# Performance work log

Hardware: AMD Instinct MI355X
Metric: run time of the kernel (lower is better)

## Reference

```python
import jax, jax.numpy as jnp
import numpy as np

B, P, F, H, C, D = 512, 32, 16, 4, 32, 128   # graphs, nodes/graph, node feat, heads, head_dim, hidden
N = B * P
E_DIM = 5

def _lin(k, o, i):
    return jax.random.normal(k, (o, i)) * (1.0 / np.sqrt(i))

def setup_inputs():
    key = jax.random.key(0)
    ks = jax.random.split(key, 32)
    # fully-connected directed edges (no self loops) within each graph
    a = np.repeat(np.arange(P), P); b = np.tile(np.arange(P), P)
    m = a != b; a, b = a[m], b[m]
    off = (np.arange(B) * P)[:, None]
    src = (a[None, :] + off).reshape(-1); dst = (b[None, :] + off).reshape(-1)
    edge_index = jnp.asarray(np.stack([src, dst]), dtype=jnp.int32)
    E = src.size
    x = jax.random.normal(ks[0], (N, F))
    edge_attr = jax.random.normal(ks[1], (E, E_DIM))
    z = jnp.zeros
    return dict(
        x=x, edge_index=edge_index, edge_attr=edge_attr,
        W1l=_lin(ks[2], D, F), b1l=z(D), W1r=_lin(ks[3], D, F), b1r=z(D),
        W1e=_lin(ks[4], D, E_DIM), att1=jax.random.normal(ks[5], (1, H, C)) * 0.1, bias1=z(D),
        W2l=_lin(ks[6], D, D), b2l=z(D), W2r=_lin(ks[7], D, D), b2r=z(D),
        W2e=_lin(ks[8], D, E_DIM), att2=jax.random.normal(ks[9], (1, H, C)) * 0.1, bias2=z(D),
        Wc1=_lin(ks[10], D, D), bc1=z(D), Wc2=_lin(ks[11], 1, D), bc2=z(1),
        Ws1=_lin(ks[12], D, D), bs1=z(D), Ws2=_lin(ks[13], 1, D), bs2=z(1),
        Wn1=_lin(ks[14], D, D), bn1=z(D), Wn2=_lin(ks[15], 1, D), bn2=z(1),
    )

def _gatv2(x, src, dst, edge_attr, Wl, bl, Wr, br, We, att, bias):
    # PyG GATv2Conv, concat=True, heads=H, out_channels=C, edge_dim=E_DIM, add_self_loops=False
    E = src.shape[0]
    xl = x @ Wl.T + bl                                   # [N, H*C] messages (source side)
    xr = x @ Wr.T + br                                   # [N, H*C] destination side
    e = (xl[src] + xr[dst] + edge_attr @ We.T).reshape(E, H, C)
    g = jax.nn.leaky_relu(e, 0.2)
    score = jnp.sum(g * att, axis=-1)                    # [E, H]
    smax = jax.ops.segment_max(score, dst, num_segments=N)
    ex = jnp.exp(score - smax[dst])
    denom = jax.ops.segment_sum(ex, dst, num_segments=N)
    alpha = ex / (denom[dst] + 1e-16)                    # segment softmax over in-edges of dst
    msg = xl[src].reshape(E, H, C) * alpha[..., None]
    return jax.ops.segment_sum(msg, dst, num_segments=N).reshape(N, H * C) + bias

def _mlp(h, W1, b1, W2, b2):
    return jax.nn.relu(h @ W1.T + b1) @ W2.T + b2

def reference(x, edge_index, edge_attr, W1l, b1l, W1r, b1r, W1e, att1, bias1,
              W2l, b2l, W2r, b2r, W2e, att2, bias2,
              Wc1, bc1, Wc2, bc2, Ws1, bs1, Ws2, bs2, Wn1, bn1, Wn2, bn2):
    src, dst = edge_index[0], edge_index[1]
    h = _gatv2(x, src, dst, edge_attr, W1l, b1l, W1r, b1r, W1e, att1, bias1)
    hb = h.reshape(B, P, D)
    h = (hb - hb.mean(axis=1, keepdims=True)).reshape(N, D)   # MeanSubtractionNorm per graph
    h = jax.nn.relu(h)
    h = jax.nn.relu(_gatv2(h, src, dst, edge_attr, W2l, b2l, W2r, b2r, W2e, att2, bias2))
    g = h.reshape(B, P, D).mean(axis=1)                       # global_mean_pool (equal-size graphs)
    value = _mlp(g, Wc1, bc1, Wc2, bc2)                       # critic        [B, 1]
    src_logits = _mlp(h, Ws1, bs1, Ws2, bs2).reshape(B, P)    # source_actor, dense per graph
    noop = _mlp(g, Wn1, bn1, Wn2, bn2)                        # noop_actor    [B, 1]
    return jnp.concatenate([value, noop, src_logits], axis=1) # [B, P+2]
```

## Files before the change

kernel.cpp:

```cpp
#include <hip/hip_runtime.h>

#define PP    32
#define FF    16
#define HH    4
#define CC    32
#define DD    128
#define EDIM  5
#define EPG   992
#define NB    512

template <int CTRL>
__device__ __forceinline__ float dpp_add(float v) {
    int t = __builtin_amdgcn_update_dpp(0, __builtin_bit_cast(int, v), CTRL, 0xF, 0xF, true);
    return v + __builtin_bit_cast(float, t);
}
__device__ __forceinline__ float red64(float v) {
    v = dpp_add<0x111>(v);
    v = dpp_add<0x112>(v);
    v = dpp_add<0x114>(v);
    v = dpp_add<0x118>(v);
    v = dpp_add<0x142>(v);
    v = dpp_add<0x143>(v);
    return v;
}
__device__ __forceinline__ float redquad(float v) {
    v = dpp_add<0xB1>(v);
    v = dpp_add<0x4E>(v);
    return v;
}

__device__ __forceinline__ void attention(const float* __restrict__ eattr,
                                          const float* __restrict__ We, const float* __restrict__ att,
                                          const float* __restrict__ bias,
                                          const float* __restrict__ sMsg, const float* __restrict__ sDst,
                                          float* __restrict__ sS, float* __restrict__ sOut,
                                          int tid, long eBase, bool relu)
{
    {
        const int s  = tid >> 4;
        const int ch0 = (tid & 15) * 8;
        float we[40], at[8], xl[8];
#pragma unroll
        for (int q = 0; q < 10; ++q)
            *(float4*)(we + q * 4) = *(const float4*)(We + ch0 * EDIM + q * 4);
        *(float4*)(at)     = *(const float4*)(att + ch0);
        *(float4*)(at + 4) = *(const float4*)(att + ch0 + 4);
        *(float4*)(xl)     = *(const float4*)(sMsg + s * DD + ch0);
        *(float4*)(xl + 4) = *(const float4*)(sMsg + s * DD + ch0 + 4);

        for (int d = 0; d < PP; ++d) {
            int jj = d - (d > s);
            if (jj > 30) jj = 30;
            const float* ea = eattr + (eBase + s * 31 + jj) * EDIM;
            const float e0 = ea[0], e1 = ea[1], e2 = ea[2], e3 = ea[3], e4 = ea[4];
            float xr[8];
            *(float4*)(xr)     = *(const float4*)(sDst + d * DD + ch0);
            *(float4*)(xr + 4) = *(const float4*)(sDst + d * DD + ch0 + 4);
            float acc0 = 0.f, acc1 = 0.f;
#pragma unroll
            for (int c = 0; c < 8; ++c) {
                float v = xl[c] + xr[c];
                const float* w = we + c * EDIM;
                v = fmaf(w[0], e0, v); v = fmaf(w[1], e1, v); v = fmaf(w[2], e2, v);
                v = fmaf(w[3], e3, v); v = fmaf(w[4], e4, v);
                v = fmaf(0.4f, fabsf(v), 0.6f * v);
                if (c & 1) acc1 = fmaf(v, at[c], acc1);
                else       acc0 = fmaf(v, at[c], acc0);
            }
            const float r = redquad(acc0 + acc1);
            if ((tid & 3) == 0)
                sS[s * DD + d * HH + ((tid >> 2) & 3)] = r;
        }
    }
    __syncthreads();
    if (tid < PP * HH) {
        const int d = tid >> 2;
        float mx = -3.4e38f;
#pragma unroll
        for (int s = 0; s < PP; ++s) if (s != d) mx = fmaxf(mx, sS[s * DD + tid]);
        float sum = 0.f;
#pragma unroll
        for (int s = 0; s < PP; ++s) {
            if (s != d) { float ex = __expf(sS[s * DD + tid] - mx); sS[s * DD + tid] = ex; sum += ex; }
        }
        const float inv = 1.f / (sum + 1e-16f);
#pragma unroll
        for (int s = 0; s < PP; ++s)
            sS[s * DD + tid] = (s == d) ? 0.f : sS[s * DD + tid] * inv;
    }
    __syncthreads();
    {
        const int d = tid >> 4, sub = tid & 15;
#pragma unroll
        for (int half = 0; half < 2; ++half) {
            const int ch4 = half * 16 + sub;
            const int idx = d * HH + (ch4 >> 3);
            const float* bp = bias + ch4 * 4;
            float4 acc = make_float4(bp[0], bp[1], bp[2], bp[3]);
#pragma unroll
            for (int s = 0; s < PP; ++s) {
                const float a = sS[s * DD + idx];
                const float4 xv = *(const float4*)(sMsg + s * DD + ch4 * 4);
                acc.x = fmaf(a, xv.x, acc.x);
                acc.y = fmaf(a, xv.y, acc.y);
                acc.z = fmaf(a, xv.z, acc.z);
                acc.w = fmaf(a, xv.w, acc.w);
            }
            if (relu) {
                acc.x = fmaxf(acc.x, 0.f); acc.y = fmaxf(acc.y, 0.f);
                acc.z = fmaxf(acc.z, 0.f); acc.w = fmaxf(acc.w, 0.f);
            }
            *(float4*)(sOut + d * DD + ch4 * 4) = acc;
        }
    }
}

extern "C" __global__ void __launch_bounds__(512, 4)
planetwars_gnn_kernel(const float* __restrict__ x, const float* __restrict__ eattr,
                      const float* __restrict__ W1l, const float* __restrict__ b1l,
                      const float* __restrict__ W1r, const float* __restrict__ b1r,
                      const float* __restrict__ W1e, const float* __restrict__ att1, const float* __restrict__ bias1,
                      const float* __restrict__ W2l, const float* __restrict__ b2l,
                      const float* __restrict__ W2r, const float* __restrict__ b2r,
                      const float* __restrict__ W2e, const float* __restrict__ att2, const float* __restrict__ bias2,
                      const float* __restrict__ Wc1, const float* __restrict__ bc1,
                      const float* __restrict__ Wc2, const float* __restrict__ bc2,
                      const float* __restrict__ Ws1, const float* __restrict__ bs1,
                      const float* __restrict__ Ws2, const float* __restrict__ bs2,
                      const float* __restrict__ Wn1, const float* __restrict__ bn1,
                      const float* __restrict__ Wn2, const float* __restrict__ bn2,
                      float* __restrict__ out)
{
    __shared__ __align__(16) float sA[PP * DD];
    __shared__ __align__(16) float sB[PP * DD];
    __shared__ __align__(16) float sH[PP * DD];
    __shared__ __align__(16) float sU[PP * DD];

    const int tid = threadIdx.x;
    const int g = blockIdx.x;
    const long eBase = (long)g * EPG;

    sU[tid] = x[g * PP * FF + tid];
    __syncthreads();

    {
        const int j = tid & 127, d0 = (tid >> 7) * 8;
        float wl[16], wr[16];
#pragma unroll
        for (int q = 0; q < 4; ++q) {
            *(float4*)(wl + q * 4) = *(const float4*)(W1l + j * FF + q * 4);
            *(float4*)(wr + q * 4) = *(const float4*)(W1r + j * FF + q * 4);
        }
        const float bl = b1l[j], br = b1r[j];
#pragma unroll
        for (int i = 0; i < 8; ++i) {
            const float* xr = sU + (d0 + i) * FF;
            float al = bl, ar = br;
#pragma unroll
            for (int k = 0; k < FF; ++k) {
                const float xv = xr[k];
                al = fmaf(wl[k], xv, al);
                ar = fmaf(wr[k], xv, ar);
            }
            sA[(d0 + i) * DD + j] = al;
            sB[(d0 + i) * DD + j] = ar;
        }
    }
    __syncthreads();

    attention(eattr, W1e, att1, bias1, sA, sB, sU, sH, tid, eBase, false);
    __syncthreads();

    if (tid < DD) {
        float s = 0.f;
#pragma unroll
        for (int d = 0; d < PP; ++d) s += sH[d * DD + tid];
        const float mn = s * (1.0f / 32.0f);
#pragma unroll
        for (int d = 0; d < PP; ++d)
            sH[d * DD + tid] = fmaxf(sH[d * DD + tid] - mn, 0.f);
    }
    __syncthreads();

    {
        const int jj = tid & 63, d0 = (tid >> 6) * 4;
        float accL0[4], accL1[4], accR0[4], accR1[4];
        const float bl0 = b2l[jj], bl1 = b2l[jj + 64];
        const float br0 = b2r[jj], br1 = b2r[jj + 64];
#pragma unroll
        for (int i = 0; i < 4; ++i) { accL0[i] = bl0; accL1[i] = bl1; accR0[i] = br0; accR1[i] = br1; }
        const float* WL0 = W2l + jj * DD;
        const float* WL1 = W2l + (jj + 64) * DD;
        const float* WR0 = W2r + jj * DD;
        const float* WR1 = W2r + (jj + 64) * DD;
        for (int k8 = 0; k8 < 16; ++k8) {
            const float4 l00 = *(const float4*)(WL0 + k8 * 8), l01 = *(const float4*)(WL0 + k8 * 8 + 4);
            const float4 l10 = *(const float4*)(WL1 + k8 * 8), l11 = *(const float4*)(WL1 + k8 * 8 + 4);
            const float4 r00 = *(const float4*)(WR0 + k8 * 8), r01 = *(const float4*)(WR0 + k8 * 8 + 4);
            const float4 r10 = *(const float4*)(WR1 + k8 * 8), r11 = *(const float4*)(WR1 + k8 * 8 + 4);
#pragma unroll
            for (int i = 0; i < 4; ++i) {
                const float4 a0 = *(const float4*)(sH + (d0 + i) * DD + k8 * 8);
                const float4 a1 = *(const float4*)(sH + (d0 + i) * DD + k8 * 8 + 4);
                accL0[i] = fmaf(l00.x, a0.x, accL0[i]); accL0[i] = fmaf(l00.y, a0.y, accL0[i]);
                accL0[i] = fmaf(l00.z, a0.z, accL0[i]); accL0[i] = fmaf(l00.w, a0.w, accL0[i]);
                accL0[i] = fmaf(l01.x, a1.x, accL0[i]); accL0[i] = fmaf(l01.y, a1.y, accL0[i]);
                accL0[i] = fmaf(l01.z, a1.z, accL0[i]); accL0[i] = fmaf(l01.w, a1.w, accL0[i]);
                accL1[i] = fmaf(l10.x, a0.x, accL1[i]); accL1[i] = fmaf(l10.y, a0.y, accL1[i]);
                accL1[i] = fmaf(l10.z, a0.z, accL1[i]); accL1[i] = fmaf(l10.w, a0.w, accL1[i]);
                accL1[i] = fmaf(l11.x, a1.x, accL1[i]); accL1[i] = fmaf(l11.y, a1.y, accL1[i]);
                accL1[i] = fmaf(l11.z, a1.z, accL1[i]); accL1[i] = fmaf(l11.w, a1.w, accL1[i]);
                accR0[i] = fmaf(r00.x, a0.x, accR0[i]); accR0[i] = fmaf(r00.y, a0.y, accR0[i]);
                accR0[i] = fmaf(r00.z, a0.z, accR0[i]); accR0[i] = fmaf(r00.w, a0.w, accR0[i]);
                accR0[i] = fmaf(r01.x, a1.x, accR0[i]); accR0[i] = fmaf(r01.y, a1.y, accR0[i]);
                accR0[i] = fmaf(r01.z, a1.z, accR0[i]); accR0[i] = fmaf(r01.w, a1.w, accR0[i]);
                accR1[i] = fmaf(r10.x, a0.x, accR1[i]); accR1[i] = fmaf(r10.y, a0.y, accR1[i]);
                accR1[i] = fmaf(r10.z, a0.z, accR1[i]); accR1[i] = fmaf(r10.w, a0.w, accR1[i]);
                accR1[i] = fmaf(r11.x, a1.x, accR1[i]); accR1[i] = fmaf(r11.y, a1.y, accR1[i]);
                accR1[i] = fmaf(r11.z, a1.z, accR1[i]); accR1[i] = fmaf(r11.w, a1.w, accR1[i]);
            }
        }
#pragma unroll
        for (int i = 0; i < 4; ++i) {
            sA[(d0 + i) * DD + jj]      = accL0[i];
            sA[(d0 + i) * DD + jj + 64] = accL1[i];
            sB[(d0 + i) * DD + jj]      = accR0[i];
            sB[(d0 + i) * DD + jj + 64] = accR1[i];
        }
    }
    __syncthreads();

    attention(eattr, W2e, att2, bias2, sA, sB, sU, sH, tid, eBase, true);
    __syncthreads();

    if (tid < DD) {
        float s = 0.f;
#pragma unroll
        for (int d = 0; d < PP; ++d) s += sH[d * DD + tid];
        sU[tid] = s * (1.0f / 32.0f);
    }
    __syncthreads();

    {
        const int jj = tid & 63, d0 = (tid >> 6) * 4;
        const float b0 = bs1[jj], b1 = bs1[jj + 64];
        float acc0[4], acc1[4];
#pragma unroll
        for (int i = 0; i < 4; ++i) { acc0[i] = b0; acc1[i] = b1; }
        const float* W0 = Ws1 + jj * DD;
        const float* W1 = Ws1 + (jj + 64) * DD;
        for (int k8 = 0; k8 < 16; ++k8) {
            const float4 w00 = *(const float4*)(W0 + k8 * 8), w01 = *(const float4*)(W0 + k8 * 8 + 4);
            const float4 w10 = *(const float4*)(W1 + k8 * 8), w11 = *(const float4*)(W1 + k8 * 8 + 4);
#pragma unroll
            for (int i = 0; i < 4; ++i) {
                const float4 a0 = *(const float4*)(sH + (d0 + i) * DD + k8 * 8);
                const float4 a1 = *(const float4*)(sH + (d0 + i) * DD + k8 * 8 + 4);
                acc0[i] = fmaf(w00.x, a0.x, acc0[i]); acc0[i] = fmaf(w00.y, a0.y, acc0[i]);
                acc0[i] = fmaf(w00.z, a0.z, acc0[i]); acc0[i] = fmaf(w00.w, a0.w, acc0[i]);
                acc0[i] = fmaf(w01.x, a1.x, acc0[i]); acc0[i] = fmaf(w01.y, a1.y, acc0[i]);
                acc0[i] = fmaf(w01.z, a1.z, acc0[i]); acc0[i] = fmaf(w01.w, a1.w, acc0[i]);
                acc1[i] = fmaf(w10.x, a0.x, acc1[i]); acc1[i] = fmaf(w10.y, a0.y, acc1[i]);
                acc1[i] = fmaf(w10.z, a0.z, acc1[i]); acc1[i] = fmaf(w10.w, a0.w, acc1[i]);
                acc1[i] = fmaf(w11.x, a1.x, acc1[i]); acc1[i] = fmaf(w11.y, a1.y, acc1[i]);
                acc1[i] = fmaf(w11.z, a1.z, acc1[i]); acc1[i] = fmaf(w11.w, a1.w, acc1[i]);
            }
        }
        const float ws2a = Ws2[jj], ws2b = Ws2[jj + 64];
        const float bias2s = bs2[0];
#pragma unroll
        for (int i = 0; i < 4; ++i) {
            const float t = fmaf(fmaxf(acc0[i], 0.f), ws2a, fmaxf(acc1[i], 0.f) * ws2b);
            const float r = red64(t);
            if ((tid & 63) == 63) out[g * 34 + 2 + d0 + i] = r + bias2s;
        }
    }

    if (tid < 128) {
        const int w = tid >> 6, j = tid & 63;
        const float* Wa = (w ? Wn1 : Wc1);
        const float* ba = (w ? bn1 : bc1);
        const float* Wb = (w ? Wn2 : Wc2);
        const float  bb = (w ? bn2 : bc2)[0];
        float h0 = ba[j], h1 = ba[j + 64];
        const float* R0 = Wa + j * DD;
        const float* R1 = Wa + (j + 64) * DD;
#pragma unroll
        for (int k8 = 0; k8 < 16; ++k8) {
            const float4 g0 = *(const float4*)(sU + k8 * 8);
            const float4 g1 = *(const float4*)(sU + k8 * 8 + 4);
            const float4 p00 = *(const float4*)(R0 + k8 * 8), p01 = *(const float4*)(R0 + k8 * 8 + 4);
            const float4 p10 = *(const float4*)(R1 + k8 * 8), p11 = *(const float4*)(R1 + k8 * 8 + 4);
            h0 = fmaf(p00.x, g0.x, h0); h0 = fmaf(p00.y, g0.y, h0);
            h0 = fmaf(p00.z, g0.z, h0); h0 = fmaf(p00.w, g0.w, h0);
            h0 = fmaf(p01.x, g1.x, h0); h0 = fmaf(p01.y, g1.y, h0);
            h0 = fmaf(p01.z, g1.z, h0); h0 = fmaf(p01.w, g1.w, h0);
            h1 = fmaf(p10.x, g0.x, h1); h1 = fmaf(p10.y, g0.y, h1);
            h1 = fmaf(p10.z, g0.z, h1); h1 = fmaf(p10.w, g0.w, h1);
            h1 = fmaf(p11.x, g1.x, h1); h1 = fmaf(p11.y, g1.y, h1);
            h1 = fmaf(p11.z, g1.z, h1); h1 = fmaf(p11.w, g1.w, h1);
        }
        const float t = fmaf(fmaxf(h0, 0.f), Wb[j], fmaxf(h1, 0.f) * Wb[j + 64]);
        const float r = red64(t);
        if (j == 63) out[g * 34 + w] = r + bb;
    }
}

extern "C" void kernel_launch(void* const* d_in, const int* in_sizes, int n_in,
                              void* d_out, int out_size, void* d_ws, size_t ws_size,
                              hipStream_t stream)
{
    (void)in_sizes; (void)n_in; (void)d_ws; (void)ws_size; (void)out_size;
    planetwars_gnn_kernel<<<dim3(NB), dim3(512), 0, stream>>>(
        (const float*)d_in[0], (const float*)d_in[2],
        (const float*)d_in[3], (const float*)d_in[4], (const float*)d_in[5], (const float*)d_in[6],
        (const float*)d_in[7], (const float*)d_in[8], (const float*)d_in[9],
        (const float*)d_in[10], (const float*)d_in[11], (const float*)d_in[12], (const float*)d_in[13],
        (const float*)d_in[14], (const float*)d_in[15], (const float*)d_in[16],
        (const float*)d_in[17], (const float*)d_in[18], (const float*)d_in[19], (const float*)d_in[20],
        (const float*)d_in[21], (const float*)d_in[22], (const float*)d_in[23], (const float*)d_in[24],
        (const float*)d_in[25], (const float*)d_in[26], (const float*)d_in[27], (const float*)d_in[28],
        (float*)d_out);
}
```

Measured before the change: 255.7 us.

## Spread softmax and column reductions over all threads with DPP quad reductions

The segment softmax and the per-graph column mean reductions now use all 512 threads, with 4 lanes per column each handling 8 rows and combining through DPP quad max/sum, where previously only 128 threads each walked 32 rows serially. The score loop is restructured so each lane loads edge attributes for one of 4 destinations and broadcasts them to its quad via DPP, and the next group's attributes are prefetched. This also removes the divergent lane-0-only score store. The aim is to cut idle threads and serial shared-memory loops, at the cost of more DPP ops and register pressure. One FMA order swap in the layer-2 GEMM is incidental.

```diff
diff --git a/kernel.cpp b/kernel.cpp
--- a/kernel.cpp
+++ b/kernel.cpp
@@ -14,6 +14,16 @@
     int t = __builtin_amdgcn_update_dpp(0, __builtin_bit_cast(int, v), CTRL, 0xF, 0xF, true);
     return v + __builtin_bit_cast(float, t);
 }
+template <int CTRL>
+__device__ __forceinline__ float dpp_mov(float v) {
+    int t = __builtin_amdgcn_update_dpp(0, __builtin_bit_cast(int, v), CTRL, 0xF, 0xF, true);
+    return __builtin_bit_cast(float, t);
+}
+template <int DK>
+__device__ __forceinline__ float qb(float v) {
+    int t = __builtin_amdgcn_update_dpp(0, __builtin_bit_cast(int, v), DK * 0x55, 0xF, 0xF, true);
+    return __builtin_bit_cast(float, t);
+}
 __device__ __forceinline__ float red64(float v) {
     v = dpp_add<0x111>(v);
     v = dpp_add<0x112>(v);
@@ -28,6 +38,35 @@
     v = dpp_add<0x4E>(v);
     return v;
 }
+__device__ __forceinline__ float maxquad(float v) {
+    v = fmaxf(v, dpp_mov<0xB1>(v));
+    v = fmaxf(v, dpp_mov<0x4E>(v));
+    return v;
+}
+
+template <int DK>
+__device__ __forceinline__ float score_step(const float* __restrict__ sDst, int d, int ch0,
+                                            const float* we, const float* at, const float* xl,
+                                            const float* eaC)
+{
+    const float e0 = qb<DK>(eaC[0]), e1 = qb<DK>(eaC[1]), e2 = qb<DK>(eaC[2]),
+                e3 = qb<DK>(eaC[3]), e4 = qb<DK>(eaC[4]);
+    float xr[8];
+    *(float4*)(xr)     = *(const float4*)(sDst + d * DD + ch0);
+    *(float4*)(xr + 4) = *(const float4*)(sDst + d * DD + ch0 + 4);
+    float acc0 = 0.f, acc1 = 0.f;
+#pragma unroll
+    for (int c = 0; c < 8; ++c) {
+        float v = xl[c] + xr[c];
+        const float* w = we + c * EDIM;
+        v = fmaf(w[0], e0, v); v = fmaf(w[1], e1, v); v = fmaf(w[2], e2, v);
+        v = fmaf(w[3], e3, v); v = fmaf(w[4], e4, v);
+        v = fmaf(0.4f, fabsf(v), 0.6f * v);
+        if (c & 1) acc1 = fmaf(v, at[c], acc1);
+        else       acc0 = fmaf(v, at[c], acc0);
+    }
+    return redquad(acc0 + acc1);
+}
 
 __device__ __forceinline__ void attention(const float* __restrict__ eattr,
                                           const float* __restrict__ We, const float* __restrict__ att,
@@ -37,7 +76,9 @@
                                           int tid, long eBase, bool relu)
 {
     {
-        const int s  = tid >> 4;
+        const int s   = tid >> 4;
+        const int h4  = (tid >> 2) & 3;
+        const int c4  = tid & 3;
         const int ch0 = (tid & 15) * 8;
         float we[40], at[8], xl[8];
 #pragma unroll
@@ -48,45 +89,62 @@
         *(float4*)(xl)     = *(const float4*)(sMsg + s * DD + ch0);
         *(float4*)(xl + 4) = *(const float4*)(sMsg + s * DD + ch0 + 4);
 
-        for (int d = 0; d < PP; ++d) {
+        float eaC[5], eaN[5];
+        {
+            const int d = c4;
             int jj = d - (d > s);
             if (jj > 30) jj = 30;
             const float* ea = eattr + (eBase + s * 31 + jj) * EDIM;
-            const float e0 = ea[0], e1 = ea[1], e2 = ea[2], e3 = ea[3], e4 = ea[4];
-            float xr[8];
-            *(float4*)(xr)     = *(const float4*)(sDst + d * DD + ch0);
-            *(float4*)(xr + 4) = *(const float4*)(sDst + d * DD + ch0 + 4);
-            float acc0 = 0.f, acc1 = 0.f;
-#pragma unroll
-            for (int c = 0; c < 8; ++c) {
-                float v = xl[c] + xr[c];
-                const float* w = we + c * EDIM;
-                v = fmaf(w[0], e0, v); v = fmaf(w[1], e1, v); v = fmaf(w[2], e2, v);
-                v = fmaf(w[3], e3, v); v = fmaf(w[4], e4, v);
-                v = fmaf(0.4f, fabsf(v), 0.6f * v);
-                if (c & 1) acc1 = fmaf(v, at[c], acc1);
-                else       acc0 = fmaf(v, at[c], acc0);
-            }
-            const float r = redquad(acc0 + acc1);
-            if ((tid & 3) == 0)
-                sS[s * DD + d * HH + ((tid >> 2) & 3)] = r;
-        }
-    }
-    __syncthreads();
-    if (tid < PP * HH) {
-        const int d = tid >> 2;
+#pragma unroll
+            for (int q = 0; q < 5; ++q) eaC[q] = ea[q];
+        }
+        for (int d0 = 0; d0 < PP; d0 += 4) {
+            {
+                int d = d0 + 4 + c4;
+                if (d > 31) d = 31;
+                int jj = d - (d > s);
+                if (jj > 30) jj = 30;
+                const float* ea = eattr + (eBase + s * 31 + jj) * EDIM;
+#pragma unroll
+                for (int q = 0; q < 5; ++q) eaN[q] = ea[q];
+            }
+            const float r0 = score_step<0>(sDst, d0 + 0, ch0, we, at, xl, eaC);
+            const float r1 = score_step<1>(sDst, d0 + 1, ch0, we, at, xl, eaC);
+            const float r2 = score_step<2>(sDst, d0 + 2, ch0, we, at, xl, eaC);
+            const float r3 = score_step<3>(sDst, d0 + 3, ch0, we, at, xl, eaC);
+            const float rw = (c4 == 0) ? r0 : (c4 == 1) ? r1 : (c4 == 2) ? r2 : r3;
+            sS[s * DD + (d0 + c4) * HH + h4] = rw;
+#pragma unroll
+            for (int q = 0; q < 5; ++q) eaC[q] = eaN[q];
+        }
+    }
+    __syncthreads();
+    {
+        const int col = tid >> 2;
+        const int r   = tid & 3;
+        const int dd  = col >> 2;
+        float v[8];
         float mx = -3.4e38f;
 #pragma unroll
-        for (int s = 0; s < PP; ++s) if (s != d) mx = fmaxf(mx, sS[s * DD + tid]);
+        for (int i = 0; i < 8; ++i) {
+            const int s = r * 8 + i;
+            v[i] = sS[s * DD + col];
+            mx = (s == dd) ? mx : fmaxf(mx, v[i]);
+        }
+        mx = maxquad(mx);
         float sum = 0.f;
 #pragma unroll
-        for (int s = 0; s < PP; ++s) {
-            if (s != d) { float ex = __expf(sS[s * DD + tid] - mx); sS[s * DD + tid] = ex; sum += ex; }
-        }
+        for (int i = 0; i < 8; ++i) {
+            const int s = r * 8 + i;
+            float ex = __expf(v[i] - mx);
+            ex = (s == dd) ? 0.f : ex;
+            v[i] = ex; sum += ex;
+        }
+        sum = redquad(sum);
         const float inv = 1.f / (sum + 1e-16f);
 #pragma unroll
-        for (int s = 0; s < PP; ++s)
-            sS[s * DD + tid] = (s == d) ? 0.f : sS[s * DD + tid] * inv;
+        for (int i = 0; i < 8; ++i)
+            sS[(r * 8 + i) * DD + col] = v[i] * inv;
     }
     __syncthreads();
     {
@@ -171,14 +229,20 @@
     attention(eattr, W1e, att1, bias1, sA, sB, sU, sH, tid, eBase, false);
     __syncthreads();
 
-    if (tid < DD) {
-        float s = 0.f;
-#pragma unroll
-        for (int d = 0; d < PP; ++d) s += sH[d * DD + tid];
-        const float mn = s * (1.0f / 32.0f);
-#pragma unroll
-        for (int d = 0; d < PP; ++d)
-            sH[d * DD + tid] = fmaxf(sH[d * DD + tid] - mn, 0.f);
+    {
+        const int col = tid >> 2, r = tid & 3;
+        float v[8];
+        float ssum = 0.f;
+#pragma unroll
+        for (int i = 0; i < 8; ++i) {
+            v[i] = sH[(r * 8 + i) * DD + col];
+            ssum += v[i];
+        }
+        ssum = redquad(ssum);
+        const float mn = ssum * (1.0f / 32.0f);
+#pragma unroll
+        for (int i = 0; i < 8; ++i)
+            sH[(r * 8 + i) * DD + col] = fmaxf(v[i] - mn, 0.f);
     }
     __syncthreads();
 
@@ -209,7 +273,7 @@
                 accL1[i] = fmaf(l10.x, a0.x, accL1[i]); accL1[i] = fmaf(l10.y, a0.y, accL1[i]);
                 accL1[i] = fmaf(l10.z, a0.z, accL1[i]); accL1[i] = fmaf(l10.w, a0.w, accL1[i]);
                 accL1[i] = fmaf(l11.x, a1.x, accL1[i]); accL1[i] = fmaf(l11.y, a1.y, accL1[i]);
-                accL1[i] = fmaf(l11.z, a1.z, accL1[i]); accL1[i] = fmaf(l11.w, a1.w, accL1[i]);
+                accL1[i] = fmaf(l11.w, a1.w, accL1[i]); accL1[i] = fmaf(l11.z, a1.z, accL1[i]);
                 accR0[i] = fmaf(r00.x, a0.x, accR0[i]); accR0[i] = fmaf(r00.y, a0.y, accR0[i]);
                 accR0[i] = fmaf(r00.z, a0.z, accR0[i]); accR0[i] = fmaf(r00.w, a0.w, accR0[i]);
                 accR0[i] = fmaf(r01.x, a1.x, accR0[i]); accR0[i] = fmaf(r01.y, a1.y, accR0[i]);
@@ -233,11 +297,13 @@
     attention(eattr, W2e, att2, bias2, sA, sB, sU, sH, tid, eBase, true);
     __syncthreads();
 
-    if (tid < DD) {
-        float s = 0.f;
-#pragma unroll
-        for (int d = 0; d < PP; ++d) s += sH[d * DD + tid];
-        sU[tid] = s * (1.0f / 32.0f);
+    {
+        const int col = tid >> 2, r = tid & 3;
+        float ssum = 0.f;
+#pragma unroll
+        for (int i = 0; i < 8; ++i) ssum += sH[(r * 8 + i) * DD + col];
+        ssum = redquad(ssum);
+        if (r == 0) sU[col] = ssum * (1.0f / 32.0f);
     }
     __syncthreads();
 
```

Measured after the change: 254.0 us. About the same (-0.6%).
